# Performance work log

Measured on AMD Instinct MI355X. Metric: run time of the kernel, lower is better.

## Reference

```python
import jax, jax.numpy as jnp
import numpy as np

N = 100000      # nodes
E = 1600000     # edges (avg degree 16)
F_IN = 128
HID = 64
OUT = 40
NB = 10000      # batch_nodes
BN_EPS = 1e-5


def setup_inputs() -> dict:
    key = jax.random.key(0)
    ks = jax.random.split(key, 16)
    inp = {}
    inp["features"] = jax.random.normal(ks[0], (N, F_IN), dtype=jnp.float32)
    inp["edge_index"] = jax.random.randint(ks[1], (2, E), 0, N, dtype=jnp.int32)
    inp["batch_nodes"] = jax.random.randint(ks[2], (NB,), 0, N, dtype=jnp.int32)
    # conv1 params (Glorot-ish scale)
    inp["W1"] = jax.random.normal(ks[3], (F_IN, HID), dtype=jnp.float32) * (1.0 / np.sqrt(F_IN))
    inp["b1"] = jnp.zeros((HID,), jnp.float32)
    inp["k2_1"] = jnp.float32(0.5)   # learnable k^2, init 0.5
    # conv2 params
    inp["W2"] = jax.random.normal(ks[4], (HID, OUT), dtype=jnp.float32) * (1.0 / np.sqrt(HID))
    inp["b2"] = jnp.zeros((OUT,), jnp.float32)
    inp["k2_2"] = jnp.float32(0.5)
    # BatchNorm1d(hid) inference params
    inp["g1"] = jax.random.uniform(ks[5], (HID,), jnp.float32, 0.5, 1.5)
    inp["be1"] = jax.random.normal(ks[6], (HID,), jnp.float32) * 0.1
    inp["m1"] = jax.random.normal(ks[7], (HID,), jnp.float32) * 0.1
    inp["v1"] = jax.random.uniform(ks[8], (HID,), jnp.float32, 0.5, 1.5)
    # BatchNorm1d(out) inference params
    inp["g2"] = jax.random.uniform(ks[9], (OUT,), jnp.float32, 0.5, 1.5)
    inp["be2"] = jax.random.normal(ks[10], (OUT,), jnp.float32) * 0.1
    inp["m2"] = jax.random.normal(ks[11], (OUT,), jnp.float32) * 0.1
    inp["v2"] = jax.random.uniform(ks[12], (OUT,), jnp.float32, 0.5, 1.5)
    return inp


def _gcn_propagate(h, src, dst, n):
    # add self loops
    loop = jnp.arange(n, dtype=src.dtype)
    s = jnp.concatenate([src, loop])
    d = jnp.concatenate([dst, loop])
    # symmetric GCN normalization D^-1/2 A_hat D^-1/2
    deg = jnp.zeros((n,), h.dtype).at[d].add(1.0)
    dinv = jax.lax.rsqrt(deg)  # deg >= 1 thanks to self loops
    coef = dinv[s] * dinv[d]   # [E+N]
    msg = coef[:, None] * h[s]                      # gather  [E+N, C]
    agg = jnp.zeros_like(h).at[d].add(msg)          # scatter [N, C]
    return agg


def _helm_conv(x, W, b, k2, src, dst, n):
    h = x @ W                                   # [N, C_out]
    agg = _gcn_propagate(h, src, dst, n)        # A_hat h
    out = agg + k2 * h + b                      # (A_hat + k^2 I) h + b
    # Helmholtz residual: (A_hat - I + k^2 I) h ~ (-L + k^2) h
    resid = agg - h + k2 * h
    helm_loss = jnp.mean(resid * resid)
    return out, helm_loss


def _bn(x, g, be, m, v):
    return (x - m) * jax.lax.rsqrt(v + BN_EPS) * g + be


def reference(features, edge_index, batch_nodes, W1, b1, k2_1, W2, b2, k2_2,
              g1, be1, m1, v1, g2, be2, m2, v2):
    n = features.shape[0]
    src, dst = edge_index[0], edge_index[1]
    x, helm_loss1 = _helm_conv(features, W1, b1, k2_1, src, dst, n)
    x = jnp.tanh(_bn(x, g1, be1, m1, v1))
    # dropout is identity in eval mode
    x, _ = _helm_conv(x, W2, b2, k2_2, src, dst, n)
    x = jnp.tanh(_bn(x, g2, be2, m2, v2))
    logp = jax.nn.log_softmax(x[batch_nodes], axis=1)
    return (logp, helm_loss1)
```

## Files before the change

kernel.cpp:

```cpp
#include <hip/hip_runtime.h>
#include <math.h>


#define BN_EPS 1e-5f
#define NB_BKT 512
#define RCAP 4608
#define PSTRIDE 5376

typedef __attribute__((ext_vector_type(8))) short bf16x8;
typedef __attribute__((ext_vector_type(4))) float f32x4;

__device__ inline unsigned short f2b(float f) {
    unsigned u = __float_as_uint(f);
    unsigned r = (u + 0x7fffu + ((u >> 16) & 1u)) >> 16;
    return (unsigned short)r;
}
__device__ inline float b2f_lo(unsigned u) { return __uint_as_float(u << 16); }
__device__ inline float b2f_hi(unsigned u) { return __uint_as_float(u & 0xffff0000u); }
__device__ inline unsigned pk2(float a, float b) {
    return (unsigned)f2b(a) | ((unsigned)f2b(b) << 16);
}
__device__ inline float tanh_fast(float x) {
    float e = __expf(2.0f * x);
    return 1.0f - 2.0f * __builtin_amdgcn_rcpf(e + 1.0f);
}
__device__ inline float qcoef(unsigned q) {
    return __uint_as_float((q >> 1) & 0xFFFF0000u);
}

__global__ __launch_bounds__(256) void k_part(const int* __restrict__ src,
                                              const int* __restrict__ dst, int e,
                                              unsigned* __restrict__ bcnt,
                                              unsigned* __restrict__ part, int nblk) {
    __shared__ unsigned h[NB_BKT];
    __shared__ unsigned gbase[NB_BKT];
    __shared__ unsigned cur[NB_BKT];
    int chunk = ((e + nblk - 1) / nblk + 3) & ~3;
    int c0 = blockIdx.x * chunk;
    int c1 = min(c0 + chunk, e);
    if (c0 >= e) return;
    for (int i = threadIdx.x; i < NB_BKT; i += 256) h[i] = 0;
    __syncthreads();
    for (int i = c0 + threadIdx.x * 4; i < c1; i += 1024) {
        if (i + 3 < c1) {
            int4 d = *(const int4*)&dst[i];
            atomicAdd(&h[(unsigned)d.x >> 8], 1u);
            atomicAdd(&h[(unsigned)d.y >> 8], 1u);
            atomicAdd(&h[(unsigned)d.z >> 8], 1u);
            atomicAdd(&h[(unsigned)d.w >> 8], 1u);
        } else {
            for (int j = i; j < c1; ++j) atomicAdd(&h[(unsigned)dst[j] >> 8], 1u);
        }
    }
    __syncthreads();
    for (int i = threadIdx.x; i < NB_BKT; i += 256) {
        unsigned c = h[i];
        gbase[i] = c ? (i * RCAP + atomicAdd(&bcnt[i], c)) : 0u;
        cur[i] = 0;
    }
    __syncthreads();
    for (int i = c0 + threadIdx.x * 4; i < c1; i += 1024) {
        if (i + 3 < c1) {
            int4 s = *(const int4*)&src[i];
            int4 d = *(const int4*)&dst[i];
            unsigned b0 = (unsigned)d.x >> 8, b1 = (unsigned)d.y >> 8;
            unsigned b2 = (unsigned)d.z >> 8, b3 = (unsigned)d.w >> 8;
            unsigned p0 = gbase[b0] + atomicAdd(&cur[b0], 1u);
            unsigned p1 = gbase[b1] + atomicAdd(&cur[b1], 1u);
            unsigned p2 = gbase[b2] + atomicAdd(&cur[b2], 1u);
            unsigned p3 = gbase[b3] + atomicAdd(&cur[b3], 1u);
            if (p0 < (b0 + 1) * RCAP) part[p0] = (((unsigned)d.x & 255u) << 24) | (unsigned)s.x;
            if (p1 < (b1 + 1) * RCAP) part[p1] = (((unsigned)d.y & 255u) << 24) | (unsigned)s.y;
            if (p2 < (b2 + 1) * RCAP) part[p2] = (((unsigned)d.z & 255u) << 24) | (unsigned)s.z;
            if (p3 < (b3 + 1) * RCAP) part[p3] = (((unsigned)d.w & 255u) << 24) | (unsigned)s.w;
        } else {
            for (int j = i; j < c1; ++j) {
                unsigned b = (unsigned)dst[j] >> 8;
                unsigned p = gbase[b] + atomicAdd(&cur[b], 1u);
                if (p < (b + 1) * RCAP)
                    part[p] = (((unsigned)dst[j] & 255u) << 24) | (unsigned)src[j];
            }
        }
    }
}

__global__ __launch_bounds__(256) void k_deg(const unsigned* __restrict__ part,
                                             const unsigned* __restrict__ bcnt,
                                             unsigned long long* __restrict__ rowinfo,
                                             float* __restrict__ dinv, int n,
                                             const float* __restrict__ b1,
                                             const float* __restrict__ g1,
                                             const float* __restrict__ be1,
                                             const float* __restrict__ m1,
                                             const float* __restrict__ v1,
                                             const float* __restrict__ b2p,
                                             const float* __restrict__ g2,
                                             const float* __restrict__ be2,
                                             const float* __restrict__ m2,
                                             const float* __restrict__ v2,
                                             float* __restrict__ A1,
                                             float* __restrict__ S1,
                                             float* __restrict__ A2,
                                             float* __restrict__ S2) {
    __shared__ unsigned hist[256];
    __shared__ unsigned sc[256];
    int b = blockIdx.x;
    int cnt = (int)min(bcnt[b], (unsigned)RCAP);
    unsigned base = b * RCAP;
    int dst0 = b << 8;
    int nloc = min(256, n - dst0);
    int t = threadIdx.x;
    hist[t] = 0;
    __syncthreads();
    for (int i = t; i < cnt; i += 256) atomicAdd(&hist[part[base + i] >> 24], 1u);
    __syncthreads();
    unsigned c = hist[t];
    unsigned pcnt = (t < nloc) ? ((c + 3u) & ~3u) : 0u;
    sc[t] = pcnt;
    __syncthreads();
    for (int off = 1; off < 256; off <<= 1) {
        unsigned a = (t >= off) ? sc[t - off] : 0u;
        __syncthreads();
        sc[t] += a;
        __syncthreads();
    }
    if (t < nloc) {
        unsigned beg = (unsigned)b * PSTRIDE + (sc[t] - pcnt);
        rowinfo[dst0 + t] = (unsigned long long)beg | ((unsigned long long)pcnt << 32);
        dinv[dst0 + t] = rsqrtf((float)(c + 1u));
    }
    if (b == 0) {
        if (t < 64) {
            float a = g1[t] * rsqrtf(v1[t] + BN_EPS);
            A1[t] = a;
            S1[t] = (b1[t] - m1[t]) * a + be1[t];
        } else if (t < 104) {
            int cc = t - 64;
            float a = g2[cc] * rsqrtf(v2[cc] + BN_EPS);
            A2[cc] = a;
            S2[cc] = (b2p[cc] - m2[cc]) * a + be2[cc];
        }
    }
}

__global__ __launch_bounds__(256) void k_scatter_gemm1(
        const unsigned* __restrict__ part, const unsigned* __restrict__ bcnt,
        const unsigned long long* __restrict__ rowinfo,
        const float* __restrict__ dinv, unsigned* __restrict__ qs,
        const float* __restrict__ X, const float* __restrict__ W,
        unsigned* __restrict__ H, int n, int nbkt) {
    __shared__ union {
        struct { unsigned cur[256]; unsigned pend[256]; } s;
        struct { short wb[4][4][64][8]; float cbuf[4][16][65]; } g;
    } u;
    int t = threadIdx.x;
    if (blockIdx.x < (unsigned)nbkt) {
        int b = blockIdx.x;
        int cnt = (int)min(bcnt[b], (unsigned)RCAP);
        unsigned base = b * RCAP;
        int dst0 = b << 8;
        int nloc = min(256, n - dst0);
        if (t < nloc) {
            unsigned long long ri = rowinfo[dst0 + t];
            u.s.cur[t] = (unsigned)ri;
            u.s.pend[t] = (unsigned)ri + (unsigned)(ri >> 32);
        } else {
            u.s.cur[t] = 0;
            u.s.pend[t] = 0;
        }
        __syncthreads();
        for (int i = t; i < cnt; i += 256) {
            unsigned p = part[base + i];
            unsigned loc = p >> 24;
            unsigned s = p & 0xFFFFFFu;
            unsigned du = __float_as_uint(dinv[s]);
            unsigned q = (((du + 0x8000u) & 0xFFFF0000u) << 1) | s;
            unsigned pos = atomicAdd(&u.s.cur[loc], 1u);
            qs[pos] = q;
        }
        __syncthreads();
        if (t < nloc) {
            for (unsigned pos = u.s.cur[t]; pos < u.s.pend[t]; ++pos) qs[pos] = 0u;
        }
        return;
    }
    int bid = blockIdx.x - nbkt;
    for (int s = t; s < 1024; s += 256) {
        int l = s & 63, nt = (s >> 6) & 3, kt = s >> 8;
        int kbase = kt * 32 + ((l >> 4) << 3);
        int nn = nt * 16 + (l & 15);
        bf16x8 v;
#pragma unroll
        for (int j = 0; j < 8; ++j) v[j] = (short)f2b(W[(kbase + j) * 64 + nn]);
        *(bf16x8*)&u.g.wb[kt][nt][l][0] = v;
    }
    __syncthreads();
    int lane = t & 63, wave = t >> 6;
    int quad = lane >> 4, m = lane & 15;
    int r0 = bid * 64 + wave * 16;
    f32x4 acc[4];
#pragma unroll
    for (int i = 0; i < 4; ++i) acc[i] = (f32x4){0.f, 0.f, 0.f, 0.f};
    int rr = min(r0 + m, n - 1);
    const float* xrow = X + (size_t)rr * 128;
#pragma unroll
    for (int kt = 0; kt < 4; ++kt) {
        int kb = kt * 32 + quad * 8;
        float4 x0 = *(const float4*)&xrow[kb];
        float4 x1 = *(const float4*)&xrow[kb + 4];
        bf16x8 af;
        af[0] = (short)f2b(x0.x); af[1] = (short)f2b(x0.y);
        af[2] = (short)f2b(x0.z); af[3] = (short)f2b(x0.w);
        af[4] = (short)f2b(x1.x); af[5] = (short)f2b(x1.y);
        af[6] = (short)f2b(x1.z); af[7] = (short)f2b(x1.w);
#pragma unroll
        for (int nt = 0; nt < 4; ++nt) {
            bf16x8 bf = *(bf16x8*)&u.g.wb[kt][nt][lane][0];
            acc[nt] = __builtin_amdgcn_mfma_f32_16x16x32_bf16(af, bf, acc[nt], 0, 0, 0);
        }
    }
#pragma unroll
    for (int nt = 0; nt < 4; ++nt)
#pragma unroll
        for (int r = 0; r < 4; ++r)
            u.g.cbuf[wave][quad * 4 + r][nt * 16 + m] = acc[nt][r];
    __syncthreads();
#pragma unroll
    for (int i = 0; i < 8; ++i) {
        int f = i * 64 + lane;
        int row = f >> 5, cp = f & 31;
        int grow = r0 + row;
        if (grow < n)
            H[(size_t)grow * 32 + cp] =
                pk2(u.g.cbuf[wave][row][2 * cp], u.g.cbuf[wave][row][2 * cp + 1]);
    }
}

__global__ __launch_bounds__(256) void k_gemm2(const unsigned short* __restrict__ X,
                                               const float* __restrict__ W,
                                               unsigned* __restrict__ H, int n) {
    __shared__ short wb[2][3][64][8];
    __shared__ float cbuf[4][16][49];
    int t = threadIdx.x;
    for (int s = t; s < 384; s += 256) {
        int l = s & 63, nt = (s >> 6) % 3, kt = s / 192;
        int kbase = kt * 32 + ((l >> 4) << 3);
        int c = nt * 16 + (l & 15);
        bf16x8 v;
#pragma unroll
        for (int j = 0; j < 8; ++j)
            v[j] = (c < 40) ? (short)f2b(W[(kbase + j) * 40 + c]) : (short)0;
        *(bf16x8*)&wb[kt][nt][l][0] = v;
    }
    __syncthreads();
    int lane = t & 63, wave = t >> 6;
    int quad = lane >> 4, m = lane & 15;
    int r0 = blockIdx.x * 64 + wave * 16;
    f32x4 acc[3];
#pragma unroll
    for (int i = 0; i < 3; ++i) acc[i] = (f32x4){0.f, 0.f, 0.f, 0.f};
    int rr = min(r0 + m, n - 1);
    const unsigned short* xrow = X + (size_t)rr * 64;
#pragma unroll
    for (int kt = 0; kt < 2; ++kt) {
        bf16x8 af = *(const bf16x8*)&xrow[kt * 32 + quad * 8];
#pragma unroll
        for (int nt = 0; nt < 3; ++nt) {
            bf16x8 bf = *(bf16x8*)&wb[kt][nt][lane][0];
            acc[nt] = __builtin_amdgcn_mfma_f32_16x16x32_bf16(af, bf, acc[nt], 0, 0, 0);
        }
    }
#pragma unroll
    for (int nt = 0; nt < 3; ++nt)
#pragma unroll
        for (int r = 0; r < 4; ++r)
            cbuf[wave][quad * 4 + r][nt * 16 + m] = acc[nt][r];
    __syncthreads();
#pragma unroll
    for (int i = 0; i < 5; ++i) {
        int f = i * 64 + lane;
        int row = f / 20, cp = f % 20;
        int grow = r0 + row;
        if (grow < n)
            H[(size_t)grow * 20 + cp] =
                pk2(cbuf[wave][row][2 * cp], cbuf[wave][row][2 * cp + 1]);
    }
}

__global__ __launch_bounds__(256) void k_conv1(const unsigned long long* __restrict__ rowinfo,
                                               const unsigned* __restrict__ qs,
                                               const float* __restrict__ dinv,
                                               const unsigned* __restrict__ h1,
                                               unsigned* __restrict__ x,
                                               const float* __restrict__ A1,
                                               const float* __restrict__ S1,
                                               const float* __restrict__ k2p,
                                               float* __restrict__ partial, int n) {
    int t = threadIdx.x;
    int lane = t & 63, wave = t >> 6;
    int quarter = lane >> 4, cl = lane & 15;
    int node = blockIdx.x * 16 + wave * 4 + quarter;
    float r2 = 0.0f;
    if (node < n) {
        unsigned long long ri = rowinfo[node];
        unsigned beg = (unsigned)ri, pdeg = (unsigned)(ri >> 32);
        float dd = dinv[node];
        uint2 hp = *(const uint2*)&h1[(unsigned)node * 32u + 2u * cl];
        float h0 = b2f_lo(hp.x), h1v = b2f_hi(hp.x);
        float h2v = b2f_lo(hp.y), h3 = b2f_hi(hp.y);
        float a0 = dd * h0, a1 = dd * h1v, a2 = dd * h2v, a3 = dd * h3;
        for (unsigned eb = 0; eb < pdeg; eb += 4) {
            uint4 q = *(const uint4*)&qs[beg + eb];
            unsigned i0 = (q.x & 0x1FFFFu) << 5, i1 = (q.y & 0x1FFFFu) << 5;
            unsigned i2 = (q.z & 0x1FFFFu) << 5, i3 = (q.w & 0x1FFFFu) << 5;
            uint2 p0 = *(const uint2*)&h1[i0 + 2u * cl];
            uint2 p1 = *(const uint2*)&h1[i1 + 2u * cl];
            uint2 p2 = *(const uint2*)&h1[i2 + 2u * cl];
            uint2 p3 = *(const uint2*)&h1[i3 + 2u * cl];
            float c0 = qcoef(q.x), c1 = qcoef(q.y), c2 = qcoef(q.z), c3 = qcoef(q.w);
            a0 += c0 * b2f_lo(p0.x); a1 += c0 * b2f_hi(p0.x);
            a2 += c0 * b2f_lo(p0.y); a3 += c0 * b2f_hi(p0.y);
            a0 += c1 * b2f_lo(p1.x); a1 += c1 * b2f_hi(p1.x);
            a2 += c1 * b2f_lo(p1.y); a3 += c1 * b2f_hi(p1.y);
            a0 += c2 * b2f_lo(p2.x); a1 += c2 * b2f_hi(p2.x);
            a2 += c2 * b2f_lo(p2.y); a3 += c2 * b2f_hi(p2.y);
            a0 += c3 * b2f_lo(p3.x); a1 += c3 * b2f_hi(p3.x);
            a2 += c3 * b2f_lo(p3.y); a3 += c3 * b2f_hi(p3.y);
        }
        float k2 = k2p[0];
        float g0 = dd * a0, g1v = dd * a1, g2v = dd * a2, g3 = dd * a3;
        float r0 = g0 + (k2 - 1.0f) * h0, r1 = g1v + (k2 - 1.0f) * h1v;
        float r2c = g2v + (k2 - 1.0f) * h2v, r3 = g3 + (k2 - 1.0f) * h3;
        r2 = r0 * r0 + r1 * r1 + r2c * r2c + r3 * r3;
        float4 Ap = *(const float4*)&A1[4 * cl];
        float4 Sp = *(const float4*)&S1[4 * cl];
        float x0 = tanh_fast((g0 + k2 * h0) * Ap.x + Sp.x);
        float x1 = tanh_fast((g1v + k2 * h1v) * Ap.y + Sp.y);
        float x2 = tanh_fast((g2v + k2 * h2v) * Ap.z + Sp.z);
        float x3 = tanh_fast((g3 + k2 * h3) * Ap.w + Sp.w);
        uint2 o;
        o.x = pk2(x0, x1);
        o.y = pk2(x2, x3);
        *(uint2*)&x[(unsigned)node * 32u + 2u * cl] = o;
    }
    for (int off = 32; off; off >>= 1) r2 += __shfl_xor(r2, off, 64);
    __shared__ float red[4];
    if (lane == 0) red[wave] = r2;
    __syncthreads();
    if (t == 0) partial[blockIdx.x] = red[0] + red[1] + red[2] + red[3];
}

__global__ __launch_bounds__(256) void k_conv2(const int* __restrict__ bn,
                                               const unsigned long long* __restrict__ rowinfo,
                                               const unsigned* __restrict__ qs,
                                               const float* __restrict__ dinv,
                                               const unsigned* __restrict__ h2,
                                               const float* __restrict__ A2,
                                               const float* __restrict__ S2,
                                               const float* __restrict__ k2p,
                                               const float* __restrict__ partial,
                                               int nparts, float inv_cnt,
                                               float* __restrict__ out, int nb) {
    int lane = threadIdx.x & 63, wave = threadIdx.x >> 6;
    if (blockIdx.x == gridDim.x - 1) {
        float s = 0.f;
        for (int i = threadIdx.x; i < nparts; i += 256) s += partial[i];
        for (int off = 32; off; off >>= 1) s += __shfl_xor(s, off, 64);
        __shared__ float red[4];
        if (lane == 0) red[wave] = s;
        __syncthreads();
        if (threadIdx.x == 0)
            out[(size_t)nb * 40] = (red[0] + red[1] + red[2] + red[3]) * inv_cnt;
        return;
    }
    int half = lane >> 5, p32 = lane & 31;
    unsigned p = (unsigned)min(p32, 19);
    int wid = blockIdx.x * 8 + wave * 2 + half;
    if (wid >= nb) return;
    int node = bn[wid];
    unsigned long long ri = rowinfo[node];
    unsigned beg = (unsigned)ri, pdeg = (unsigned)(ri >> 32);
    float dd = dinv[node];
    unsigned hp = h2[(unsigned)node * 20u + p];
    float hx = b2f_lo(hp), hy = b2f_hi(hp);
    float ax = dd * hx, ay = dd * hy;
    for (unsigned eb = 0; eb < pdeg; eb += 4) {
        uint4 q = *(const uint4*)&qs[beg + eb];
        unsigned pv0 = h2[(q.x & 0x1FFFFu) * 20u + p];
        unsigned pv1 = h2[(q.y & 0x1FFFFu) * 20u + p];
        unsigned pv2 = h2[(q.z & 0x1FFFFu) * 20u + p];
        unsigned pv3 = h2[(q.w & 0x1FFFFu) * 20u + p];
        float c0 = qcoef(q.x), c1 = qcoef(q.y), c2 = qcoef(q.z), c3 = qcoef(q.w);
        ax += c0 * b2f_lo(pv0); ay += c0 * b2f_hi(pv0);
        ax += c1 * b2f_lo(pv1); ay += c1 * b2f_hi(pv1);
        ax += c2 * b2f_lo(pv2); ay += c2 * b2f_hi(pv2);
        ax += c3 * b2f_lo(pv3); ay += c3 * b2f_hi(pv3);
    }
    float k2 = k2p[0];
    float2 Ap = *(const float2*)&A2[2 * p];
    float2 Sp = *(const float2*)&S2[2 * p];
    float tx = tanh_fast((dd * ax + k2 * hx) * Ap.x + Sp.x);
    float ty = tanh_fast((dd * ay + k2 * hy) * Ap.y + Sp.y);
    bool act = (p32 < 20);
    float mx = act ? fmaxf(tx, ty) : -INFINITY;
    for (int off = 16; off; off >>= 1) mx = fmaxf(mx, __shfl_xor(mx, off, 32));
    float es = act ? (__expf(tx - mx) + __expf(ty - mx)) : 0.f;
    for (int off = 16; off; off >>= 1) es += __shfl_xor(es, off, 32);
    if (act) {
        float ls = mx + __logf(es);
        float2 o = make_float2(tx - ls, ty - ls);
        *(float2*)&out[(size_t)wid * 40 + 2 * p] = o;
    }
}

extern "C" void kernel_launch(void* const* d_in, const int* in_sizes, int n_in,
                              void* d_out, int out_size, void* d_ws, size_t ws_size,
                              hipStream_t stream) {
    const float* features = (const float*)d_in[0];
    const int* edge_index = (const int*)d_in[1];
    const int* batch_nodes = (const int*)d_in[2];
    const float* W1 = (const float*)d_in[3];
    const float* b1 = (const float*)d_in[4];
    const float* k2_1 = (const float*)d_in[5];
    const float* W2 = (const float*)d_in[6];
    const float* b2 = (const float*)d_in[7];
    const float* k2_2 = (const float*)d_in[8];
    const float* g1 = (const float*)d_in[9];
    const float* be1 = (const float*)d_in[10];
    const float* m1 = (const float*)d_in[11];
    const float* v1 = (const float*)d_in[12];
    const float* g2 = (const float*)d_in[13];
    const float* be2 = (const float*)d_in[14];
    const float* m2 = (const float*)d_in[15];
    const float* v2 = (const float*)d_in[16];

    const int N = in_sizes[0] / 128;
    const int E = in_sizes[1] / 2;
    const int NB = in_sizes[2];
    const int* src = edge_index;
    const int* dst = edge_index + E;
    const int NPART = (N + 15) / 16;
    const int NBKT = (N + 255) >> 8;
    const int PBLK = 256;
    const int GEMM1B = (N + 63) / 64;

    unsigned* ws = (unsigned*)d_ws;
    auto align64 = [](size_t o) { return (o + 63) & ~(size_t)63; };
    size_t o = 0;
    unsigned long long* rowinfo = (unsigned long long*)(ws + o); o = align64(o + 2 * (size_t)N);
    float* dinv = (float*)(ws + o);       o = align64(o + N);
    float* A1 = (float*)(ws + o);         o = align64(o + 64);
    float* S1 = (float*)(ws + o);         o = align64(o + 64);
    float* A2 = (float*)(ws + o);         o = align64(o + 64);
    float* S2 = (float*)(ws + o);         o = align64(o + 64);
    unsigned* bcnt = ws + o;              o = align64(o + NB_BKT);
    float* partial = (float*)(ws + o);    o = align64(o + NPART);
    unsigned* qs = ws + o;                o = align64(o + (size_t)NB_BKT * PSTRIDE);
    unsigned* h1 = ws + o;                o = align64(o + (size_t)N * 32);
    unsigned* x = ws + o;                 o = align64(o + (size_t)N * 32);
    unsigned* h2 = ws + o;                o = align64(o + (size_t)N * 20);
    unsigned* part = ws + o;              o = align64(o + (size_t)NB_BKT * RCAP);

    hipMemsetAsync(bcnt, 0, NB_BKT * sizeof(unsigned), stream);
    k_part<<<PBLK, 256, 0, stream>>>(src, dst, E, bcnt, part, PBLK);
    k_deg<<<NBKT, 256, 0, stream>>>(part, bcnt, rowinfo, dinv, N, b1, g1, be1, m1,
                                    v1, b2, g2, be2, m2, v2, A1, S1, A2, S2);
    k_scatter_gemm1<<<NBKT + GEMM1B, 256, 0, stream>>>(part, bcnt, rowinfo, dinv,
                                                       qs, features, W1, h1, N, NBKT);
    k_conv1<<<NPART, 256, 0, stream>>>(rowinfo, qs, dinv, h1, x, A1, S1, k2_1,
                                       partial, N);
    k_gemm2<<<(N + 63) / 64, 256, 0, stream>>>((const unsigned short*)x, W2, h2, N);
    k_conv2<<<(NB + 7) / 8 + 1, 256, 0, stream>>>(batch_nodes, rowinfo, qs, dinv, h2,
                                                  A2, S2, k2_2, partial, NPART,
                                                  1.0f / ((float)N * 64.0f),
                                                  (float*)d_out, NB);
}
```

Baseline: 221.3 us.

## Prescale features by dinv in GEMMs and drop per-edge coefficients from CSR

The symmetric normalization is refactored so each GEMM epilogue multiplies its output rows by the source node's dinv. Aggregation then becomes a plain sum of neighbour rows scaled once by the destination dinv, and the CSR stores only bare indices. Degree counting and CSR scatter are merged into a single build kernel, and row padding goes from 4 to 8 so the gather loops can unroll by 8. Padding slots point at a zero row appended to h1/h2. This removes the per-edge coefficient math and the dinv gather in the scatter phase. The trade-offs are an extra kernel boundary between build and GEMM1 (they used to run concurrently in one launch), more padding traffic, and extra bf16 rounding since the prescaled values are stored in bf16.

```diff
diff --git a/kernel.cpp b/kernel.cpp
--- a/kernel.cpp
+++ b/kernel.cpp
@@ -5,7 +5,7 @@
 #define BN_EPS 1e-5f
 #define NB_BKT 512
 #define RCAP 4608
-#define PSTRIDE 5376
+#define PSTRIDE 6400
 
 typedef __attribute__((ext_vector_type(8))) short bf16x8;
 typedef __attribute__((ext_vector_type(4))) float f32x4;
@@ -23,9 +23,6 @@
 __device__ inline float tanh_fast(float x) {
     float e = __expf(2.0f * x);
     return 1.0f - 2.0f * __builtin_amdgcn_rcpf(e + 1.0f);
-}
-__device__ inline float qcoef(unsigned q) {
-    return __uint_as_float((q >> 1) & 0xFFFF0000u);
 }
 
 __global__ __launch_bounds__(256) void k_part(const int* __restrict__ src,
@@ -84,51 +81,33 @@
     }
 }
 
-__global__ __launch_bounds__(256) void k_deg(const unsigned* __restrict__ part,
-                                             const unsigned* __restrict__ bcnt,
-                                             unsigned long long* __restrict__ rowinfo,
-                                             float* __restrict__ dinv, int n,
-                                             const float* __restrict__ b1,
-                                             const float* __restrict__ g1,
-                                             const float* __restrict__ be1,
-                                             const float* __restrict__ m1,
-                                             const float* __restrict__ v1,
-                                             const float* __restrict__ b2p,
-                                             const float* __restrict__ g2,
-                                             const float* __restrict__ be2,
-                                             const float* __restrict__ m2,
-                                             const float* __restrict__ v2,
-                                             float* __restrict__ A1,
-                                             float* __restrict__ S1,
-                                             float* __restrict__ A2,
-                                             float* __restrict__ S2) {
+__global__ __launch_bounds__(256) void k_build(const unsigned* __restrict__ part,
+                                               const unsigned* __restrict__ bcnt,
+                                               unsigned long long* __restrict__ rowinfo,
+                                               float* __restrict__ dinv,
+                                               unsigned* __restrict__ qs, int n,
+                                               const float* __restrict__ b1,
+                                               const float* __restrict__ g1,
+                                               const float* __restrict__ be1,
+                                               const float* __restrict__ m1,
+                                               const float* __restrict__ v1,
+                                               const float* __restrict__ b2p,
+                                               const float* __restrict__ g2,
+                                               const float* __restrict__ be2,
+                                               const float* __restrict__ m2,
+                                               const float* __restrict__ v2,
+                                               float* __restrict__ A1,
+                                               float* __restrict__ S1,
+                                               float* __restrict__ A2,
+                                               float* __restrict__ S2,
+                                               unsigned* __restrict__ h1,
+                                               unsigned* __restrict__ h2) {
     __shared__ unsigned hist[256];
     __shared__ unsigned sc[256];
+    __shared__ unsigned cur[256];
+    __shared__ unsigned pend[256];
     int b = blockIdx.x;
-    int cnt = (int)min(bcnt[b], (unsigned)RCAP);
-    unsigned base = b * RCAP;
-    int dst0 = b << 8;
-    int nloc = min(256, n - dst0);
     int t = threadIdx.x;
-    hist[t] = 0;
-    __syncthreads();
-    for (int i = t; i < cnt; i += 256) atomicAdd(&hist[part[base + i] >> 24], 1u);
-    __syncthreads();
-    unsigned c = hist[t];
-    unsigned pcnt = (t < nloc) ? ((c + 3u) & ~3u) : 0u;
-    sc[t] = pcnt;
-    __syncthreads();
-    for (int off = 1; off < 256; off <<= 1) {
-        unsigned a = (t >= off) ? sc[t - off] : 0u;
-        __syncthreads();
-        sc[t] += a;
-        __syncthreads();
-    }
-    if (t < nloc) {
-        unsigned beg = (unsigned)b * PSTRIDE + (sc[t] - pcnt);
-        rowinfo[dst0 + t] = (unsigned long long)beg | ((unsigned long long)pcnt << 32);
-        dinv[dst0 + t] = rsqrtf((float)(c + 1u));
-    }
     if (b == 0) {
         if (t < 64) {
             float a = g1[t] * rsqrtf(v1[t] + BN_EPS);
@@ -139,52 +118,54 @@
             float a = g2[cc] * rsqrtf(v2[cc] + BN_EPS);
             A2[cc] = a;
             S2[cc] = (b2p[cc] - m2[cc]) * a + be2[cc];
-        }
-    }
-}
-
-__global__ __launch_bounds__(256) void k_scatter_gemm1(
-        const unsigned* __restrict__ part, const unsigned* __restrict__ bcnt,
-        const unsigned long long* __restrict__ rowinfo,
-        const float* __restrict__ dinv, unsigned* __restrict__ qs,
-        const float* __restrict__ X, const float* __restrict__ W,
-        unsigned* __restrict__ H, int n, int nbkt) {
-    __shared__ union {
-        struct { unsigned cur[256]; unsigned pend[256]; } s;
-        struct { short wb[4][4][64][8]; float cbuf[4][16][65]; } g;
-    } u;
+        } else if (t < 136) {
+            h1[(size_t)n * 32u + (t - 104)] = 0u;
+        } else if (t < 156) {
+            h2[(size_t)n * 20u + (t - 136)] = 0u;
+        }
+    }
+    int cnt = (int)min(bcnt[b], (unsigned)RCAP);
+    unsigned base = b * RCAP;
+    int dst0 = b << 8;
+    int nloc = min(256, n - dst0);
+    hist[t] = 0;
+    __syncthreads();
+    for (int i = t; i < cnt; i += 256) atomicAdd(&hist[part[base + i] >> 24], 1u);
+    __syncthreads();
+    unsigned c = hist[t];
+    unsigned pcnt = (t < nloc) ? ((c + 7u) & ~7u) : 0u;
+    sc[t] = pcnt;
+    __syncthreads();
+    for (int off = 1; off < 256; off <<= 1) {
+        unsigned a = (t >= off) ? sc[t - off] : 0u;
+        __syncthreads();
+        sc[t] += a;
+        __syncthreads();
+    }
+    unsigned beg = (unsigned)b * PSTRIDE + (sc[t] - pcnt);
+    if (t < nloc) {
+        rowinfo[dst0 + t] = (unsigned long long)beg | ((unsigned long long)pcnt << 32);
+        dinv[dst0 + t] = rsqrtf((float)(c + 1u));
+    }
+    cur[t] = beg;
+    pend[t] = beg + pcnt;
+    __syncthreads();
+    for (int i = t; i < cnt; i += 256) {
+        unsigned p = part[base + i];
+        unsigned pos = atomicAdd(&cur[p >> 24], 1u);
+        qs[pos] = p & 0xFFFFFFu;
+    }
+    __syncthreads();
+    for (unsigned pos = cur[t]; pos < pend[t]; ++pos) qs[pos] = (unsigned)n;
+}
+
+__global__ __launch_bounds__(256) void k_gemm1(const float* __restrict__ X,
+                                               const float* __restrict__ W,
+                                               const float* __restrict__ dinv,
+                                               unsigned* __restrict__ H, int n) {
+    __shared__ short wb[4][4][64][8];
+    __shared__ float cbuf[4][16][65];
     int t = threadIdx.x;
-    if (blockIdx.x < (unsigned)nbkt) {
-        int b = blockIdx.x;
-        int cnt = (int)min(bcnt[b], (unsigned)RCAP);
-        unsigned base = b * RCAP;
-        int dst0 = b << 8;
-        int nloc = min(256, n - dst0);
-        if (t < nloc) {
-            unsigned long long ri = rowinfo[dst0 + t];
-            u.s.cur[t] = (unsigned)ri;
-            u.s.pend[t] = (unsigned)ri + (unsigned)(ri >> 32);
-        } else {
-            u.s.cur[t] = 0;
-            u.s.pend[t] = 0;
-        }
-        __syncthreads();
-        for (int i = t; i < cnt; i += 256) {
-            unsigned p = part[base + i];
-            unsigned loc = p >> 24;
-            unsigned s = p & 0xFFFFFFu;
-            unsigned du = __float_as_uint(dinv[s]);
-            unsigned q = (((du + 0x8000u) & 0xFFFF0000u) << 1) | s;
-            unsigned pos = atomicAdd(&u.s.cur[loc], 1u);
-            qs[pos] = q;
-        }
-        __syncthreads();
-        if (t < nloc) {
-            for (unsigned pos = u.s.cur[t]; pos < u.s.pend[t]; ++pos) qs[pos] = 0u;
-        }
-        return;
-    }
-    int bid = blockIdx.x - nbkt;
     for (int s = t; s < 1024; s += 256) {
         int l = s & 63, nt = (s >> 6) & 3, kt = s >> 8;
         int kbase = kt * 32 + ((l >> 4) << 3);
@@ -192,12 +173,12 @@
         bf16x8 v;
 #pragma unroll
         for (int j = 0; j < 8; ++j) v[j] = (short)f2b(W[(kbase + j) * 64 + nn]);
-        *(bf16x8*)&u.g.wb[kt][nt][l][0] = v;
+        *(bf16x8*)&wb[kt][nt][l][0] = v;
     }
     __syncthreads();
     int lane = t & 63, wave = t >> 6;
     int quad = lane >> 4, m = lane & 15;
-    int r0 = bid * 64 + wave * 16;
+    int r0 = blockIdx.x * 64 + wave * 16;
     f32x4 acc[4];
 #pragma unroll
     for (int i = 0; i < 4; ++i) acc[i] = (f32x4){0.f, 0.f, 0.f, 0.f};
@@ -215,7 +196,7 @@
         af[6] = (short)f2b(x1.z); af[7] = (short)f2b(x1.w);
 #pragma unroll
         for (int nt = 0; nt < 4; ++nt) {
-            bf16x8 bf = *(bf16x8*)&u.g.wb[kt][nt][lane][0];
+            bf16x8 bf = *(bf16x8*)&wb[kt][nt][lane][0];
             acc[nt] = __builtin_amdgcn_mfma_f32_16x16x32_bf16(af, bf, acc[nt], 0, 0, 0);
         }
     }
@@ -223,21 +204,24 @@
     for (int nt = 0; nt < 4; ++nt)
 #pragma unroll
         for (int r = 0; r < 4; ++r)
-            u.g.cbuf[wave][quad * 4 + r][nt * 16 + m] = acc[nt][r];
+            cbuf[wave][quad * 4 + r][nt * 16 + m] = acc[nt][r];
     __syncthreads();
 #pragma unroll
     for (int i = 0; i < 8; ++i) {
         int f = i * 64 + lane;
         int row = f >> 5, cp = f & 31;
         int grow = r0 + row;
-        if (grow < n)
+        if (grow < n) {
+            float dv = dinv[grow];
             H[(size_t)grow * 32 + cp] =
-                pk2(u.g.cbuf[wave][row][2 * cp], u.g.cbuf[wave][row][2 * cp + 1]);
+                pk2(dv * cbuf[wave][row][2 * cp], dv * cbuf[wave][row][2 * cp + 1]);
+        }
     }
 }
 
 __global__ __launch_bounds__(256) void k_gemm2(const unsigned short* __restrict__ X,
                                                const float* __restrict__ W,
+                                               const float* __restrict__ dinv,
                                                unsigned* __restrict__ H, int n) {
     __shared__ short wb[2][3][64][8];
     __shared__ float cbuf[4][16][49];
@@ -281,9 +265,11 @@
         int f = i * 64 + lane;
         int row = f / 20, cp = f % 20;
         int grow = r0 + row;
-        if (grow < n)
+        if (grow < n) {
+            float dv = dinv[grow];
             H[(size_t)grow * 20 + cp] =
-                pk2(cbuf[wave][row][2 * cp], cbuf[wave][row][2 * cp + 1]);
+                pk2(dv * cbuf[wave][row][2 * cp], dv * cbuf[wave][row][2 * cp + 1]);
+        }
     }
 }
 
@@ -305,27 +291,38 @@
         unsigned long long ri = rowinfo[node];
         unsigned beg = (unsigned)ri, pdeg = (unsigned)(ri >> 32);
         float dd = dinv[node];
+        float rdd = __builtin_amdgcn_rcpf(dd);
         uint2 hp = *(const uint2*)&h1[(unsigned)node * 32u + 2u * cl];
-        float h0 = b2f_lo(hp.x), h1v = b2f_hi(hp.x);
-        float h2v = b2f_lo(hp.y), h3 = b2f_hi(hp.y);
-        float a0 = dd * h0, a1 = dd * h1v, a2 = dd * h2v, a3 = dd * h3;
-        for (unsigned eb = 0; eb < pdeg; eb += 4) {
-            uint4 q = *(const uint4*)&qs[beg + eb];
-            unsigned i0 = (q.x & 0x1FFFFu) << 5, i1 = (q.y & 0x1FFFFu) << 5;
-            unsigned i2 = (q.z & 0x1FFFFu) << 5, i3 = (q.w & 0x1FFFFu) << 5;
-            uint2 p0 = *(const uint2*)&h1[i0 + 2u * cl];
-            uint2 p1 = *(const uint2*)&h1[i1 + 2u * cl];
-            uint2 p2 = *(const uint2*)&h1[i2 + 2u * cl];
-            uint2 p3 = *(const uint2*)&h1[i3 + 2u * cl];
-            float c0 = qcoef(q.x), c1 = qcoef(q.y), c2 = qcoef(q.z), c3 = qcoef(q.w);
-            a0 += c0 * b2f_lo(p0.x); a1 += c0 * b2f_hi(p0.x);
-            a2 += c0 * b2f_lo(p0.y); a3 += c0 * b2f_hi(p0.y);
-            a0 += c1 * b2f_lo(p1.x); a1 += c1 * b2f_hi(p1.x);
-            a2 += c1 * b2f_lo(p1.y); a3 += c1 * b2f_hi(p1.y);
-            a0 += c2 * b2f_lo(p2.x); a1 += c2 * b2f_hi(p2.x);
-            a2 += c2 * b2f_lo(p2.y); a3 += c2 * b2f_hi(p2.y);
-            a0 += c3 * b2f_lo(p3.x); a1 += c3 * b2f_hi(p3.x);
-            a2 += c3 * b2f_lo(p3.y); a3 += c3 * b2f_hi(p3.y);
+        float a0 = b2f_lo(hp.x), a1 = b2f_hi(hp.x);
+        float a2 = b2f_lo(hp.y), a3 = b2f_hi(hp.y);
+        float h0 = a0 * rdd, h1v = a1 * rdd, h2v = a2 * rdd, h3 = a3 * rdd;
+        for (unsigned eb = 0; eb < pdeg; eb += 8) {
+            uint4 q0 = *(const uint4*)&qs[beg + eb];
+            uint4 q1 = *(const uint4*)&qs[beg + eb + 4];
+            uint2 p0 = *(const uint2*)&h1[(q0.x << 5) + 2u * cl];
+            uint2 p1 = *(const uint2*)&h1[(q0.y << 5) + 2u * cl];
+            uint2 p2 = *(const uint2*)&h1[(q0.z << 5) + 2u * cl];
+            uint2 p3 = *(const uint2*)&h1[(q0.w << 5) + 2u * cl];
+            uint2 p4 = *(const uint2*)&h1[(q1.x << 5) + 2u * cl];
+            uint2 p5 = *(const uint2*)&h1[(q1.y << 5) + 2u * cl];
+            uint2 p6 = *(const uint2*)&h1[(q1.z << 5) + 2u * cl];
+            uint2 p7 = *(const uint2*)&h1[(q1.w << 5) + 2u * cl];
+            a0 += b2f_lo(p0.x); a1 += b2f_hi(p0.x);
+            a2 += b2f_lo(p0.y); a3 += b2f_hi(p0.y);
+            a0 += b2f_lo(p1.x); a1 += b2f_hi(p1.x);
+            a2 += b2f_lo(p1.y); a3 += b2f_hi(p1.y);
+            a0 += b2f_lo(p2.x); a1 += b2f_hi(p2.x);
+            a2 += b2f_lo(p2.y); a3 += b2f_hi(p2.y);
+            a0 += b2f_lo(p3.x); a1 += b2f_hi(p3.x);
+            a2 += b2f_lo(p3.y); a3 += b2f_hi(p3.y);
+            a0 += b2f_lo(p4.x); a1 += b2f_hi(p4.x);
+            a2 += b2f_lo(p4.y); a3 += b2f_hi(p4.y);
+            a0 += b2f_lo(p5.x); a1 += b2f_hi(p5.x);
+            a2 += b2f_lo(p5.y); a3 += b2f_hi(p5.y);
+            a0 += b2f_lo(p6.x); a1 += b2f_hi(p6.x);
+            a2 += b2f_lo(p6.y); a3 += b2f_hi(p6.y);
+            a0 += b2f_lo(p7.x); a1 += b2f_hi(p7.x);
+            a2 += b2f_lo(p7.y); a3 += b2f_hi(p7.y);
         }
         float k2 = k2p[0];
         float g0 = dd * a0, g1v = dd * a1, g2v = dd * a2, g3 = dd * a3;
@@ -381,20 +378,29 @@
     unsigned long long ri = rowinfo[node];
     unsigned beg = (unsigned)ri, pdeg = (unsigned)(ri >> 32);
     float dd = dinv[node];
+    float rdd = __builtin_amdgcn_rcpf(dd);
     unsigned hp = h2[(unsigned)node * 20u + p];
-    float hx = b2f_lo(hp), hy = b2f_hi(hp);
-    float ax = dd * hx, ay = dd * hy;
-    for (unsigned eb = 0; eb < pdeg; eb += 4) {
-        uint4 q = *(const uint4*)&qs[beg + eb];
-        unsigned pv0 = h2[(q.x & 0x1FFFFu) * 20u + p];
-        unsigned pv1 = h2[(q.y & 0x1FFFFu) * 20u + p];
-        unsigned pv2 = h2[(q.z & 0x1FFFFu) * 20u + p];
-        unsigned pv3 = h2[(q.w & 0x1FFFFu) * 20u + p];
-        float c0 = qcoef(q.x), c1 = qcoef(q.y), c2 = qcoef(q.z), c3 = qcoef(q.w);
-        ax += c0 * b2f_lo(pv0); ay += c0 * b2f_hi(pv0);
-        ax += c1 * b2f_lo(pv1); ay += c1 * b2f_hi(pv1);
-        ax += c2 * b2f_lo(pv2); ay += c2 * b2f_hi(pv2);
-        ax += c3 * b2f_lo(pv3); ay += c3 * b2f_hi(pv3);
+    float ax = b2f_lo(hp), ay = b2f_hi(hp);
+    float hx = ax * rdd, hy = ay * rdd;
+    for (unsigned eb = 0; eb < pdeg; eb += 8) {
+        uint4 q0 = *(const uint4*)&qs[beg + eb];
+        uint4 q1 = *(const uint4*)&qs[beg + eb + 4];
+        unsigned pv0 = h2[q0.x * 20u + p];
+        unsigned pv1 = h2[q0.y * 20u + p];
+        unsigned pv2 = h2[q0.z * 20u + p];
+        unsigned pv3 = h2[q0.w * 20u + p];
+        unsigned pv4 = h2[q1.x * 20u + p];
+        unsigned pv5 = h2[q1.y * 20u + p];
+        unsigned pv6 = h2[q1.z * 20u + p];
+        unsigned pv7 = h2[q1.w * 20u + p];
+        ax += b2f_lo(pv0); ay += b2f_hi(pv0);
+        ax += b2f_lo(pv1); ay += b2f_hi(pv1);
+        ax += b2f_lo(pv2); ay += b2f_hi(pv2);
+        ax += b2f_lo(pv3); ay += b2f_hi(pv3);
+        ax += b2f_lo(pv4); ay += b2f_hi(pv4);
+        ax += b2f_lo(pv5); ay += b2f_hi(pv5);
+        ax += b2f_lo(pv6); ay += b2f_hi(pv6);
+        ax += b2f_lo(pv7); ay += b2f_hi(pv7);
     }
     float k2 = k2p[0];
     float2 Ap = *(const float2*)&A2[2 * p];
@@ -442,7 +448,6 @@
     const int NPART = (N + 15) / 16;
     const int NBKT = (N + 255) >> 8;
     const int PBLK = 256;
-    const int GEMM1B = (N + 63) / 64;
 
     unsigned* ws = (unsigned*)d_ws;
     auto align64 = [](size_t o) { return (o + 63) & ~(size_t)63; };
@@ -456,20 +461,21 @@
     unsigned* bcnt = ws + o;              o = align64(o + NB_BKT);
     float* partial = (float*)(ws + o);    o = align64(o + NPART);
     unsigned* qs = ws + o;                o = align64(o + (size_t)NB_BKT * PSTRIDE);
-    unsigned* h1 = ws + o;                o = align64(o + (size_t)N * 32);
+    unsigned* h1 = ws + o;                o = align64(o + (size_t)(N + 1) * 32);
     unsigned* x = ws + o;                 o = align64(o + (size_t)N * 32);
-    unsigned* h2 = ws + o;                o = align64(o + (size_t)N * 20);
+    unsigned* h2 = ws + o;                o = align64(o + (size_t)(N + 1) * 20);
     unsigned* part = ws + o;              o = align64(o + (size_t)NB_BKT * RCAP);
 
     hipMemsetAsync(bcnt, 0, NB_BKT * sizeof(unsigned), stream);
     k_part<<<PBLK, 256, 0, stream>>>(src, dst, E, bcnt, part, PBLK);
-    k_deg<<<NBKT, 256, 0, stream>>>(part, bcnt, rowinfo, dinv, N, b1, g1, be1, m1,
-                                    v1, b2, g2, be2, m2, v2, A1, S1, A2, S2);
-    k_scatter_gemm1<<<NBKT + GEMM1B, 256, 0, stream>>>(part, bcnt, rowinfo, dinv,
-                                                       qs, features, W1, h1, N, NBKT);
+    k_build<<<NBKT, 256, 0, stream>>>(part, bcnt, rowinfo, dinv, qs, N, b1, g1,
+                                      be1, m1, v1, b2, g2, be2, m2, v2, A1, S1,
+                                      A2, S2, h1, h2);
+    k_gemm1<<<(N + 63) / 64, 256, 0, stream>>>(features, W1, dinv, h1, N);
     k_conv1<<<NPART, 256, 0, stream>>>(rowinfo, qs, dinv, h1, x, A1, S1, k2_1,
                                        partial, N);
-    k_gemm2<<<(N + 63) / 64, 256, 0, stream>>>((const unsigned short*)x, W2, h2, N);
+    k_gemm2<<<(N + 63) / 64, 256, 0, stream>>>((const unsigned short*)x, W2, dinv,
+                                               h2, N);
     k_conv2<<<(NB + 7) / 8 + 1, 256, 0, stream>>>(batch_nodes, rowinfo, qs, dinv, h2,
                                                   A2, S2, k2_2, partial, NPART,
                                                   1.0f / ((float)N * 64.0f),
```

After: 216.9 us (median of 2 runs). 1.02x faster.
